# Optimization experiments

Hardware: AMD Instinct MI355X
Metric: run time of the kernel (lower is better)

Reference implementation:

```python
import jax, jax.numpy as jnp
import numpy as np

MARGIN = 1.0

def setup_inputs() -> dict:
    key = jax.random.key(0)
    k1, k2 = jax.random.split(key)
    score = jax.random.normal(k1, (4096, 128), dtype=jnp.float32)
    target = jax.random.randint(k2, (4096,), 0, 64, dtype=jnp.int64)
    return {"score": score, "target": target}

def reference(score, target):
    # Pairwise squared distances: ||x_i||^2 + ||x_j||^2 - 2 x_i . x_j
    mag = jnp.sum(score * score, axis=1)                       # [B]
    sim = jnp.einsum('id,jd->ij', score, score)                # [B,B]
    d2 = jax.nn.relu(mag[:, None] + mag[None, :] - 2.0 * sim)  # [B,B]
    # safe sqrt (double-where) so masked-out zeros don't poison grads
    pos_d2 = d2 > 0.0
    dist = jnp.where(pos_d2, jnp.sqrt(jnp.where(pos_d2, d2, 1.0)), 0.0)

    same = target[:, None] == target[None, :]                  # [B,B]
    # negative-pair row sums: sum_{j: t_j != t_i} exp(margin - d_ij)
    neg_exp = jnp.where(~same, jnp.exp(MARGIN - dist), 0.0)
    neg_sum = jnp.sum(neg_exp, axis=1)                         # [B]

    B = score.shape[0]
    upper = jnp.triu(jnp.ones((B, B), dtype=bool), k=1)
    pos_mask = same & upper                                    # same-class pairs, i<j

    l_n = jnp.log(neg_sum[:, None] + neg_sum[None, :])         # [B,B]
    per_pair = jax.nn.relu(l_n + dist) ** 2
    loss_sum = jnp.sum(jnp.where(pos_mask, per_pair, 0.0))
    counter = jnp.maximum(jnp.sum(pos_mask), 1)
    return loss_sum / (2.0 * counter.astype(score.dtype))
```

## Files before the change

kernel.cpp:

```cpp
#include <hip/hip_runtime.h>
#include <hip/hip_bf16.h>

#define BN 4096
#define DD 128
#define SD 136
#define NCLS 64
#define MARGIN_F 1.0f
#define NTRI 528
#define NSLOT 64

typedef __attribute__((ext_vector_type(8))) short bf16x8;
typedef __attribute__((ext_vector_type(4))) float f32x4;

__device__ __forceinline__ unsigned short f2bf(float f) {
    __hip_bfloat16 h = __float2bfloat16(f);
    return *reinterpret_cast<unsigned short*>(&h);
}

__global__ __launch_bounds__(256) void prep_kernel(
    const float* __restrict__ score,
    unsigned short* __restrict__ sbf,
    float* __restrict__ mag,
    int* __restrict__ tail)
{
    const int tid = threadIdx.x;
    const int w = tid >> 6, lane = tid & 63;
    const int row = blockIdx.x * 8 + w * 2 + (lane >> 5);
    const int l32 = lane & 31;
    if (blockIdx.x == 0 && tid == 0) *tail = 0;
    float4 v = *reinterpret_cast<const float4*>(score + (size_t)row * DD + l32 * 4);
    ushort4 u;
    u.x = f2bf(v.x); u.y = f2bf(v.y); u.z = f2bf(v.z); u.w = f2bf(v.w);
    *reinterpret_cast<ushort4*>(sbf + (size_t)row * SD + l32 * 4) = u;
    float s = v.x * v.x + v.y * v.y + v.z * v.z + v.w * v.w;
    #pragma unroll
    for (int o = 16; o > 0; o >>= 1) s += __shfl_xor(s, o);
    if (l32 == 0) mag[row] = s;
}

__global__ __launch_bounds__(256, 2) void negsum_kernel(
    const unsigned short* __restrict__ sbf,
    const float* __restrict__ mag,
    const int* __restrict__ tgt,
    float* __restrict__ negp)
{
    const int idx = blockIdx.x;
    const int tid = threadIdx.x;
    const int wid = tid >> 6, lane = tid & 63;
    const int lhi = lane >> 4, llo = lane & 15;
    const int wr = wid >> 1, wc = wid & 1;

    int bi = (int)((65.0f - __builtin_amdgcn_sqrtf(4225.0f - 8.0f * (float)idx)) * 0.5f);
    bi = max(0, min(bi, 31));
    while (bi * (65 - bi) / 2 > idx) --bi;
    while ((bi + 1) * (64 - bi) / 2 <= idx) ++bi;
    const int bj = bi + (idx - bi * (65 - bi) / 2);
    const bool diag = (bi == bj);

    const int i0 = bi * 128 + wr * 64;
    const int j0 = bj * 128 + wc * 64;

    f32x4 acc[4][4] = {};
    #pragma unroll
    for (int kk = 0; kk < 4; ++kk) {
        const int koff = kk * 32 + lhi * 8;
        bf16x8 a[4], b[4];
        #pragma unroll
        for (int m = 0; m < 4; ++m)
            a[m] = *reinterpret_cast<const bf16x8*>(sbf + (size_t)(i0 + m * 16 + llo) * SD + koff);
        #pragma unroll
        for (int n = 0; n < 4; ++n)
            b[n] = *reinterpret_cast<const bf16x8*>(sbf + (size_t)(j0 + n * 16 + llo) * SD + koff);
        #pragma unroll
        for (int m = 0; m < 4; ++m)
            #pragma unroll
            for (int n = 0; n < 4; ++n)
                acc[m][n] = __builtin_amdgcn_mfma_f32_16x16x32_bf16(a[m], b[n], acc[m][n], 0, 0, 0);
    }

    float magj[4]; int tj[4];
    #pragma unroll
    for (int n = 0; n < 4; ++n) {
        const int j = j0 + n * 16 + llo;
        magj[n] = mag[j];
        tj[n] = tgt[j];
    }

    float cs[4] = {0.0f, 0.0f, 0.0f, 0.0f};
    const int rslot = bj * 2 + wc;
    #pragma unroll
    for (int m = 0; m < 4; ++m) {
        const int ibase = i0 + m * 16 + lhi * 4;
        f32x4 magi = *reinterpret_cast<const f32x4*>(mag + ibase);
        int4 ti4 = *reinterpret_cast<const int4*>(tgt + ibase);
        const int* tip = &ti4.x;
        f32x4 rs = {0.0f, 0.0f, 0.0f, 0.0f};
        #pragma unroll
        for (int r = 0; r < 4; ++r) {
            const int ti = tip[r];
            float s = 0.0f;
            #pragma unroll
            for (int n = 0; n < 4; ++n) {
                float d2 = fmaxf(magi[r] + magj[n] - 2.0f * acc[m][n][r], 0.0f);
                float dist = __builtin_amdgcn_sqrtf(d2);
                float v = (ti != tj[n]) ? __expf(MARGIN_F - dist) : 0.0f;
                s += v;
                cs[n] += v;
            }
            #pragma unroll
            for (int o = 1; o < 16; o <<= 1) s += __shfl_xor(s, o);
            rs[r] = s;
        }
        if (llo == 0) {
            #pragma unroll
            for (int r = 0; r < 4; ++r)
                negp[(size_t)(ibase + r) * NSLOT + rslot] = rs[r];
        }
    }

    if (!diag) {
        #pragma unroll
        for (int n = 0; n < 4; ++n) {
            cs[n] += __shfl_xor(cs[n], 16);
            cs[n] += __shfl_xor(cs[n], 32);
        }
        const int cslot = bi * 2 + wr;
        if (lhi == 0) {
            #pragma unroll
            for (int n = 0; n < 4; ++n)
                negp[(size_t)(j0 + n * 16 + llo) * NSLOT + cslot] = cs[n];
        }
    }
}

__global__ __launch_bounds__(256) void loss_kernel(
    const unsigned short* __restrict__ sbf,
    const float* __restrict__ mag,
    const float* __restrict__ negp,
    const int* __restrict__ tgt,
    float2* __restrict__ part,
    int* __restrict__ tail,
    float* __restrict__ out)
{
    const int c = blockIdx.x;
    const int tid = threadIdx.x;
    const int wid = tid >> 6, lane = tid & 63;

    __shared__ int slist[256];
    __shared__ int wsum[4];
    __shared__ int snc;
    __shared__ float sneg[256];
    int4 tv[4];
    #pragma unroll
    for (int k = 0; k < 4; ++k)
        tv[k] = *reinterpret_cast<const int4*>(tgt + tid * 16 + k * 4);
    int cnt = 0;
    #pragma unroll
    for (int k = 0; k < 4; ++k) {
        const int* q = &tv[k].x;
        #pragma unroll
        for (int e = 0; e < 4; ++e) cnt += (q[e] == c) ? 1 : 0;
    }
    int inc = cnt;
    #pragma unroll
    for (int o = 1; o < 64; o <<= 1) {
        int u = __shfl_up(inc, o);
        if (lane >= o) inc += u;
    }
    if (lane == 63) wsum[wid] = inc;
    __syncthreads();
    int wpre = 0;
    #pragma unroll
    for (int w = 0; w < 4; ++w) wpre += (w < wid) ? wsum[w] : 0;
    if (tid == 255) snc = wpre + inc;
    int pos = wpre + inc - cnt;
    #pragma unroll
    for (int k = 0; k < 4; ++k) {
        const int* q = &tv[k].x;
        #pragma unroll
        for (int e = 0; e < 4; ++e) {
            if (q[e] == c && pos < 256) { slist[pos] = tid * 16 + k * 4 + e; ++pos; }
        }
    }
    __syncthreads();
    const int n_c = snc;

    if (tid < n_c) {
        const f32x4* p = reinterpret_cast<const f32x4*>(negp + (size_t)slist[tid] * NSLOT);
        f32x4 s4 = {0.0f, 0.0f, 0.0f, 0.0f};
        #pragma unroll
        for (int k = 0; k < 16; ++k) {
            f32x4 v = p[k];
            s4[0] += v[0]; s4[1] += v[1]; s4[2] += v[2]; s4[3] += v[3];
        }
        sneg[tid] = (s4[0] + s4[1]) + (s4[2] + s4[3]);
    }
    __syncthreads();

    const int wr = wid >> 1, wc = wid & 1;
    const int p0 = wr * 64, q0 = wc * 64;
    const int lhi = lane >> 4, llo = lane & 15;

    float lsum = 0.0f, lcnt = 0.0f;
    const bool active = (n_c > 0) && (wc >= wr) && (p0 < n_c) && (q0 < n_c);
    if (active) {
        int opA[4], opB[4], qcl[4];
        #pragma unroll
        for (int m = 0; m < 4; ++m)
            opA[m] = slist[min(p0 + m * 16 + llo, n_c - 1)];
        #pragma unroll
        for (int n = 0; n < 4; ++n) {
            qcl[n] = min(q0 + n * 16 + llo, n_c - 1);
            opB[n] = slist[qcl[n]];
        }

        f32x4 acc[4][4] = {};
        #pragma unroll
        for (int kk = 0; kk < 4; ++kk) {
            const int koff = kk * 32 + lhi * 8;
            bf16x8 a[4], b[4];
            #pragma unroll
            for (int m = 0; m < 4; ++m)
                a[m] = *reinterpret_cast<const bf16x8*>(sbf + (size_t)opA[m] * SD + koff);
            #pragma unroll
            for (int n = 0; n < 4; ++n)
                b[n] = *reinterpret_cast<const bf16x8*>(sbf + (size_t)opB[n] * SD + koff);
            #pragma unroll
            for (int m = 0; m < 4; ++m)
                #pragma unroll
                for (int n = 0; n < 4; ++n)
                    acc[m][n] = __builtin_amdgcn_mfma_f32_16x16x32_bf16(a[m], b[n], acc[m][n], 0, 0, 0);
        }

        float magjv[4], nsj[4]; int qv[4];
        #pragma unroll
        for (int n = 0; n < 4; ++n) {
            qv[n] = q0 + n * 16 + llo;
            magjv[n] = mag[opB[n]];
            nsj[n] = sneg[qcl[n]];
        }

        #pragma unroll
        for (int m = 0; m < 4; ++m) {
            #pragma unroll
            for (int r = 0; r < 4; ++r) {
                const int p = p0 + m * 16 + lhi * 4 + r;
                const bool pv = (p < n_c);
                const int pcl = min(p, n_c - 1);
                const int io = slist[pcl];
                const float magiv = mag[io];
                const float nsi = sneg[pcl];
                #pragma unroll
                for (int n = 0; n < 4; ++n) {
                    if (pv && qv[n] > p && qv[n] < n_c) {
                        float d2 = fmaxf(magiv + magjv[n] - 2.0f * acc[m][n][r], 0.0f);
                        float dist = __builtin_amdgcn_sqrtf(d2);
                        float ln = __logf(nsi + nsj[n]);
                        float uu = fmaxf(ln + dist, 0.0f);
                        lsum += uu * uu;
                        lcnt += 1.0f;
                    }
                }
            }
        }
    }

    #pragma unroll
    for (int o = 32; o > 0; o >>= 1) {
        lsum += __shfl_xor(lsum, o);
        lcnt += __shfl_xor(lcnt, o);
    }
    __shared__ float2 wpart[4];
    __shared__ int dlast;
    if (lane == 0) wpart[wid] = make_float2(lsum, lcnt);
    __syncthreads();
    if (tid == 0) {
        float s = 0.0f, cc = 0.0f;
        #pragma unroll
        for (int w = 0; w < 4; ++w) { s += wpart[w].x; cc += wpart[w].y; }
        part[c] = make_float2(s, cc);
        __threadfence();
        dlast = (atomicAdd(tail, 1) == NCLS - 1) ? 1 : 0;
    }
    __syncthreads();
    if (dlast && tid < 64) {
        __threadfence();
        float2 p = part[lane];
        float s = p.x, cc = p.y;
        #pragma unroll
        for (int o = 32; o > 0; o >>= 1) {
            s += __shfl_xor(s, o);
            cc += __shfl_xor(cc, o);
        }
        if (lane == 0) out[0] = s / (2.0f * fmaxf(cc, 1.0f));
    }
}

extern "C" void kernel_launch(void* const* d_in, const int* in_sizes, int n_in,
                              void* d_out, int out_size, void* d_ws, size_t ws_size,
                              hipStream_t stream) {
    const float* score = (const float*)d_in[0];
    const int* tgt = (const int*)d_in[1];
    float* out = (float*)d_out;

    char* ws = (char*)d_ws;
    unsigned short* sbf = (unsigned short*)ws;
    float* mag = (float*)(ws + (size_t)BN * SD * 2 + 64);
    float* negp = mag + BN;
    float2* part = (float2*)(negp + (size_t)BN * NSLOT);
    int* tail = (int*)(part + NCLS);

    prep_kernel<<<512, 256, 0, stream>>>(score, sbf, mag, tail);
    negsum_kernel<<<NTRI, 256, 0, stream>>>(sbf, mag, tgt, negp);
    loss_kernel<<<NCLS, 256, 0, stream>>>(sbf, mag, negp, tgt, part, tail, out);
}
```

Measured before the change: 36.56 us.

## Fuse negsum and loss kernels via ticket counter and spin-wait

Merges the negative-sum and loss kernels into one launch. Each of the 528 blocks takes a ticket after its negsum tile; the last 64 ticket holders become per-class loss blocks and spin until all tiles are done. This removes one kernel launch boundary and its tail gap. The cost is a grid-wide spin dependency, which relies on all blocks being co-resident or scheduled. It also carries the loss kernel's state under the negsum launch bounds.

```diff
diff --git a/kernel.cpp b/kernel.cpp
--- a/kernel.cpp
+++ b/kernel.cpp
@@ -27,7 +27,7 @@
     const int w = tid >> 6, lane = tid & 63;
     const int row = blockIdx.x * 8 + w * 2 + (lane >> 5);
     const int l32 = lane & 31;
-    if (blockIdx.x == 0 && tid == 0) *tail = 0;
+    if (blockIdx.x == 0 && tid < 2) tail[tid] = 0;
     float4 v = *reinterpret_cast<const float4*>(score + (size_t)row * DD + l32 * 4);
     ushort4 u;
     u.x = f2bf(v.x); u.y = f2bf(v.y); u.z = f2bf(v.z); u.w = f2bf(v.w);
@@ -38,11 +38,14 @@
     if (l32 == 0) mag[row] = s;
 }
 
-__global__ __launch_bounds__(256, 2) void negsum_kernel(
+__global__ __launch_bounds__(256, 2) void mega_kernel(
     const unsigned short* __restrict__ sbf,
     const float* __restrict__ mag,
     const int* __restrict__ tgt,
-    float* __restrict__ negp)
+    float* __restrict__ negp,
+    float2* __restrict__ part,
+    int* __restrict__ tail,
+    float* __restrict__ out)
 {
     const int idx = blockIdx.x;
     const int tid = threadIdx.x;
@@ -50,101 +53,105 @@
     const int lhi = lane >> 4, llo = lane & 15;
     const int wr = wid >> 1, wc = wid & 1;
 
-    int bi = (int)((65.0f - __builtin_amdgcn_sqrtf(4225.0f - 8.0f * (float)idx)) * 0.5f);
-    bi = max(0, min(bi, 31));
-    while (bi * (65 - bi) / 2 > idx) --bi;
-    while ((bi + 1) * (64 - bi) / 2 <= idx) ++bi;
-    const int bj = bi + (idx - bi * (65 - bi) / 2);
-    const bool diag = (bi == bj);
-
-    const int i0 = bi * 128 + wr * 64;
-    const int j0 = bj * 128 + wc * 64;
-
-    f32x4 acc[4][4] = {};
-    #pragma unroll
-    for (int kk = 0; kk < 4; ++kk) {
-        const int koff = kk * 32 + lhi * 8;
-        bf16x8 a[4], b[4];
-        #pragma unroll
-        for (int m = 0; m < 4; ++m)
-            a[m] = *reinterpret_cast<const bf16x8*>(sbf + (size_t)(i0 + m * 16 + llo) * SD + koff);
-        #pragma unroll
-        for (int n = 0; n < 4; ++n)
-            b[n] = *reinterpret_cast<const bf16x8*>(sbf + (size_t)(j0 + n * 16 + llo) * SD + koff);
-        #pragma unroll
-        for (int m = 0; m < 4; ++m)
+    {
+        int bi = (int)((65.0f - __builtin_amdgcn_sqrtf(4225.0f - 8.0f * (float)idx)) * 0.5f);
+        bi = max(0, min(bi, 31));
+        while (bi * (65 - bi) / 2 > idx) --bi;
+        while ((bi + 1) * (64 - bi) / 2 <= idx) ++bi;
+        const int bj = bi + (idx - bi * (65 - bi) / 2);
+        const bool diag = (bi == bj);
+
+        const int i0 = bi * 128 + wr * 64;
+        const int j0 = bj * 128 + wc * 64;
+
+        f32x4 acc[4][4] = {};
+        #pragma unroll
+        for (int kk = 0; kk < 4; ++kk) {
+            const int koff = kk * 32 + lhi * 8;
+            bf16x8 a[4], b[4];
+            #pragma unroll
+            for (int m = 0; m < 4; ++m)
+                a[m] = *reinterpret_cast<const bf16x8*>(sbf + (size_t)(i0 + m * 16 + llo) * SD + koff);
             #pragma unroll
             for (int n = 0; n < 4; ++n)
-                acc[m][n] = __builtin_amdgcn_mfma_f32_16x16x32_bf16(a[m], b[n], acc[m][n], 0, 0, 0);
-    }
-
-    float magj[4]; int tj[4];
-    #pragma unroll
-    for (int n = 0; n < 4; ++n) {
-        const int j = j0 + n * 16 + llo;
-        magj[n] = mag[j];
-        tj[n] = tgt[j];
-    }
-
-    float cs[4] = {0.0f, 0.0f, 0.0f, 0.0f};
-    const int rslot = bj * 2 + wc;
-    #pragma unroll
-    for (int m = 0; m < 4; ++m) {
-        const int ibase = i0 + m * 16 + lhi * 4;
-        f32x4 magi = *reinterpret_cast<const f32x4*>(mag + ibase);
-        int4 ti4 = *reinterpret_cast<const int4*>(tgt + ibase);
-        const int* tip = &ti4.x;
-        f32x4 rs = {0.0f, 0.0f, 0.0f, 0.0f};
-        #pragma unroll
-        for (int r = 0; r < 4; ++r) {
-            const int ti = tip[r];
-            float s = 0.0f;
+                b[n] = *reinterpret_cast<const bf16x8*>(sbf + (size_t)(j0 + n * 16 + llo) * SD + koff);
+            #pragma unroll
+            for (int m = 0; m < 4; ++m)
+                #pragma unroll
+                for (int n = 0; n < 4; ++n)
+                    acc[m][n] = __builtin_amdgcn_mfma_f32_16x16x32_bf16(a[m], b[n], acc[m][n], 0, 0, 0);
+        }
+
+        float magj[4]; int tj[4];
+        #pragma unroll
+        for (int n = 0; n < 4; ++n) {
+            const int j = j0 + n * 16 + llo;
+            magj[n] = mag[j];
+            tj[n] = tgt[j];
+        }
+
+        float cs[4] = {0.0f, 0.0f, 0.0f, 0.0f};
+        const int rslot = bj * 2 + wc;
+        #pragma unroll
+        for (int m = 0; m < 4; ++m) {
+            const int ibase = i0 + m * 16 + lhi * 4;
+            f32x4 magi = *reinterpret_cast<const f32x4*>(mag + ibase);
+            int4 ti4 = *reinterpret_cast<const int4*>(tgt + ibase);
+            const int* tip = &ti4.x;
+            f32x4 rs = {0.0f, 0.0f, 0.0f, 0.0f};
+            #pragma unroll
+            for (int r = 0; r < 4; ++r) {
+                const int ti = tip[r];
+                float s = 0.0f;
+                #pragma unroll
+                for (int n = 0; n < 4; ++n) {
+                    float d2 = fmaxf(magi[r] + magj[n] - 2.0f * acc[m][n][r], 0.0f);
+                    float dist = __builtin_amdgcn_sqrtf(d2);
+                    float v = (ti != tj[n]) ? __expf(MARGIN_F - dist) : 0.0f;
+                    s += v;
+                    cs[n] += v;
+                }
+                #pragma unroll
+                for (int o = 1; o < 16; o <<= 1) s += __shfl_xor(s, o);
+                rs[r] = s;
+            }
+            if (llo == 0) {
+                #pragma unroll
+                for (int r = 0; r < 4; ++r)
+                    negp[(size_t)(ibase + r) * NSLOT + rslot] = rs[r];
+            }
+        }
+
+        if (!diag) {
             #pragma unroll
             for (int n = 0; n < 4; ++n) {
-                float d2 = fmaxf(magi[r] + magj[n] - 2.0f * acc[m][n][r], 0.0f);
-                float dist = __builtin_amdgcn_sqrtf(d2);
-                float v = (ti != tj[n]) ? __expf(MARGIN_F - dist) : 0.0f;
-                s += v;
-                cs[n] += v;
-            }
-            #pragma unroll
-            for (int o = 1; o < 16; o <<= 1) s += __shfl_xor(s, o);
-            rs[r] = s;
-        }
-        if (llo == 0) {
-            #pragma unroll
-            for (int r = 0; r < 4; ++r)
-                negp[(size_t)(ibase + r) * NSLOT + rslot] = rs[r];
-        }
-    }
-
-    if (!diag) {
-        #pragma unroll
-        for (int n = 0; n < 4; ++n) {
-            cs[n] += __shfl_xor(cs[n], 16);
-            cs[n] += __shfl_xor(cs[n], 32);
-        }
-        const int cslot = bi * 2 + wr;
-        if (lhi == 0) {
-            #pragma unroll
-            for (int n = 0; n < 4; ++n)
-                negp[(size_t)(j0 + n * 16 + llo) * NSLOT + cslot] = cs[n];
-        }
-    }
-}
-
-__global__ __launch_bounds__(256) void loss_kernel(
-    const unsigned short* __restrict__ sbf,
-    const float* __restrict__ mag,
-    const float* __restrict__ negp,
-    const int* __restrict__ tgt,
-    float2* __restrict__ part,
-    int* __restrict__ tail,
-    float* __restrict__ out)
-{
-    const int c = blockIdx.x;
-    const int tid = threadIdx.x;
-    const int wid = tid >> 6, lane = tid & 63;
+                cs[n] += __shfl_xor(cs[n], 16);
+                cs[n] += __shfl_xor(cs[n], 32);
+            }
+            const int cslot = bi * 2 + wr;
+            if (lhi == 0) {
+                #pragma unroll
+                for (int n = 0; n < 4; ++n)
+                    negp[(size_t)(j0 + n * 16 + llo) * NSLOT + cslot] = cs[n];
+            }
+        }
+    }
+
+    __shared__ int sticket;
+    __threadfence();
+    __syncthreads();
+    if (tid == 0) sticket = atomicAdd(&tail[0], 1);
+    __syncthreads();
+    const int ticket = sticket;
+    if (ticket < NTRI - NCLS) return;
+    const int c = ticket - (NTRI - NCLS);
+
+    if (tid == 0) {
+        while (__hip_atomic_load(&tail[0], __ATOMIC_ACQUIRE, __HIP_MEMORY_SCOPE_AGENT) < NTRI)
+            __builtin_amdgcn_s_sleep(1);
+    }
+    __syncthreads();
+    __threadfence();
 
     __shared__ int slist[256];
     __shared__ int wsum[4];
@@ -197,9 +204,7 @@
     }
     __syncthreads();
 
-    const int wr = wid >> 1, wc = wid & 1;
     const int p0 = wr * 64, q0 = wc * 64;
-    const int lhi = lane >> 4, llo = lane & 15;
 
     float lsum = 0.0f, lcnt = 0.0f;
     const bool active = (n_c > 0) && (wc >= wr) && (p0 < n_c) && (q0 < n_c);
@@ -280,7 +285,7 @@
         for (int w = 0; w < 4; ++w) { s += wpart[w].x; cc += wpart[w].y; }
         part[c] = make_float2(s, cc);
         __threadfence();
-        dlast = (atomicAdd(tail, 1) == NCLS - 1) ? 1 : 0;
+        dlast = (atomicAdd(&tail[1], 1) == NCLS - 1) ? 1 : 0;
     }
     __syncthreads();
     if (dlast && tid < 64) {
@@ -311,6 +316,5 @@
     int* tail = (int*)(part + NCLS);
 
     prep_kernel<<<512, 256, 0, stream>>>(score, sbf, mag, tail);
-    negsum_kernel<<<NTRI, 256, 0, stream>>>(sbf, mag, tgt, negp);
-    loss_kernel<<<NCLS, 256, 0, stream>>>(sbf, mag, negp, tgt, part, tail, out);
+    mega_kernel<<<NTRI, 256, 0, stream>>>(sbf, mag, tgt, negp, part, tail, out);
 }
```

After: 132.5 us, median of 2. +262.3%, slower.
